# Optimization experiments

Measured on AMD Instinct MI355X. Metric: run time of the kernel, lower is better.

## Reference

```python
import jax, jax.numpy as jnp
import numpy as np

N_NODES = 50000
N_EDGES = 600000
DIM = 128
GROUPS = 32  # min(32, dim)
EPS = 1e-5


def setup_inputs() -> dict:
    key = jax.random.key(0)
    ks = jax.random.split(key, 10)
    src = jax.random.randint(ks[0], (N_EDGES,), 0, N_NODES)
    tgt = jax.random.randint(ks[1], (N_EDGES,), 0, N_NODES)
    # normalized adjacency values (Mtgt): mean aggregation 1/deg(tgt)
    deg = jax.ops.segment_sum(jnp.ones((N_EDGES,), jnp.float32), tgt, num_segments=N_NODES)
    edge_w = 1.0 / jnp.maximum(deg, 1.0)[tgt]
    x = jax.random.normal(ks[2], (N_NODES, DIM), jnp.float32)
    t = jax.random.uniform(ks[3], (), jnp.float32)
    sc = 1.0 / np.sqrt(DIM + 1)
    W1 = jax.random.normal(ks[4], (DIM + 1, DIM), jnp.float32) * sc
    b1 = jax.random.normal(ks[5], (DIM,), jnp.float32) * 0.01
    W2 = jax.random.normal(ks[6], (DIM + 1, DIM), jnp.float32) * sc
    b2 = jax.random.normal(ks[7], (DIM,), jnp.float32) * 0.01
    return {
        "t": t, "x": x, "src": src, "tgt": tgt, "edge_w": edge_w,
        "W1": W1, "b1": b1, "W2": W2, "b2": b2,
        "gamma1": jnp.ones((DIM,), jnp.float32), "beta1": jnp.zeros((DIM,), jnp.float32),
        "gamma2": jnp.ones((DIM,), jnp.float32), "beta2": jnp.zeros((DIM,), jnp.float32),
    }


def _group_norm(h, gamma, beta):
    n, c = h.shape
    hg = h.reshape(n, GROUPS, c // GROUPS)
    mu = hg.mean(axis=-1, keepdims=True)
    var = hg.var(axis=-1, keepdims=True)
    hn = ((hg - mu) * jax.lax.rsqrt(var + EPS)).reshape(n, c)
    return hn * gamma + beta


def _gconv(ttx, W, b, src, tgt, edge_w):
    s = ttx @ W + b                      # [N, dim] projected support
    msg = s[src] * edge_w[:, None]       # [E, dim] gathered, adj-weighted messages
    return jax.ops.segment_sum(msg, tgt, num_segments=N_NODES)


def reference(t, x, src, tgt, edge_w, W1, b1, W2, b2, gamma1, beta1, gamma2, beta2):
    tt = jnp.full((x.shape[0], 1), 1.0, x.dtype) * t
    ttx = jnp.concatenate([tt, x], axis=1)
    h = jax.nn.relu(_gconv(ttx, W1, b1, src, tgt, edge_w))
    h = _group_norm(h, gamma1, beta1)
    ttx = jnp.concatenate([tt, h], axis=1)
    h = jax.nn.relu(_gconv(ttx, W2, b2, src, tgt, edge_w))
    h = _group_norm(h, gamma2, beta2)
    return h
```

## Files before the change

kernel.cpp:

```cpp
#include <hip/hip_runtime.h>
#include <hip/hip_bf16.h>

#define N_NODES 50000
#define N_EDGES 600000
#define DIM 128
#define EPS 1e-5f

#define NPB 64
#define GEMM_GRID ((N_NODES + NPB - 1) / NPB)
#define HIST_BLOCKS 512
#define NSLICE 8
#define GPB 256
#define SCAN_NB 49

typedef float  f32x4   __attribute__((ext_vector_type(4)));
typedef short  s16x8   __attribute__((ext_vector_type(8)));
typedef unsigned short u16x4 __attribute__((ext_vector_type(4)));

__device__ __forceinline__ unsigned short f2b(float f) {
    unsigned int u = __float_as_uint(f);
    return (unsigned short)((u + 0x7fffu + ((u >> 16) & 1u)) >> 16);
}
__device__ __forceinline__ float b2f(unsigned short h) {
    return __uint_as_float(((unsigned int)h) << 16);
}

__device__ __forceinline__ void gemm_body(
    const float* __restrict__ xin, const float* __restrict__ W,
    const float* __restrict__ bias, const float* __restrict__ tptr,
    float* __restrict__ sout, int tile, char* lds)
{
    char* ah = lds;
    char* al = lds + 8192;
    char* wh = lds + 16384;
    char* wl = lds + 32768;

    const int tid  = threadIdx.x;
    const int nb   = tile * NPB;
    const int lane = tid & 63;
    const int wv   = tid >> 6;
    const int g    = lane >> 4;
    const int c16  = lane & 15;

    const float4* xin4 = (const float4*)xin;
    const float4* w4   = (const float4*)(W + DIM);

    f32x4 acc[4][2];
#pragma unroll
    for (int m = 0; m < 4; ++m)
#pragma unroll
        for (int n = 0; n < 2; ++n)
            acc[m][n] = (f32x4){0.f, 0.f, 0.f, 0.f};

#pragma unroll 1
    for (int kt = 0; kt < 2; ++kt) {
        if (kt) __syncthreads();

#pragma unroll
        for (int i = 0; i < 4; ++i) {
            int f4 = tid + i * 256;
            int nl = f4 >> 4;
            int q  = f4 & 15;
            int node = nb + nl;
            float4 v = make_float4(0.f, 0.f, 0.f, 0.f);
            if (node < N_NODES) v = xin4[(size_t)node * 32 + kt * 16 + q];
            unsigned short h0 = f2b(v.x), h1 = f2b(v.y), h2 = f2b(v.z), h3 = f2b(v.w);
            unsigned short l0 = f2b(v.x - b2f(h0)), l1 = f2b(v.y - b2f(h1));
            unsigned short l2 = f2b(v.z - b2f(h2)), l3 = f2b(v.w - b2f(h3));
            int byt = (nl * 128 + q * 8) ^ ((nl & 7) << 4);
            *(u16x4*)(ah + byt) = (u16x4){h0, h1, h2, h3};
            *(u16x4*)(al + byt) = (u16x4){l0, l1, l2, l3};
        }
#pragma unroll
        for (int i = 0; i < 8; ++i) {
            int f4 = tid + i * 256;
            int kr = f4 >> 5;
            int c4 = f4 & 31;
            float4 v = w4[(size_t)(kt * 64 + kr) * 32 + c4];
            unsigned short h0 = f2b(v.x), h1 = f2b(v.y), h2 = f2b(v.z), h3 = f2b(v.w);
            unsigned short l0 = f2b(v.x - b2f(h0)), l1 = f2b(v.y - b2f(h1));
            unsigned short l2 = f2b(v.z - b2f(h2)), l3 = f2b(v.w - b2f(h3));
            int cc = c4 >> 2, cq = c4 & 3;
            int byt = (cc * 2048 + kr * 32 + cq * 8) ^ (((kr >> 3) & 3) << 5);
            *(u16x4*)(wh + byt) = (u16x4){h0, h1, h2, h3};
            *(u16x4*)(wl + byt) = (u16x4){l0, l1, l2, l3};
        }
        __syncthreads();

#pragma unroll
        for (int ks = 0; ks < 2; ++ks) {
            const int k0 = ks * 32;
            s16x8 Ah[4], Al[4];
#pragma unroll
            for (int m = 0; m < 4; ++m) {
                int node = m * 16 + c16;
                int byt = (node * 128 + ks * 64 + g * 16) ^ ((node & 7) << 4);
                Ah[m] = *(const s16x8*)(ah + byt);
                Al[m] = *(const s16x8*)(al + byt);
            }
            s16x8 Bh[2], Bl[2];
#pragma unroll
            for (int n = 0; n < 2; ++n) {
                int cc = wv * 2 + n;
                int sw = ((((k0 >> 3) + g) & 3) << 5);
                int fb = cc * 2048 + (k0 + g * 8) * 32 + c16 * 2;
#pragma unroll
                for (int j = 0; j < 8; ++j) {
                    int a = (fb + j * 32) ^ sw;
                    Bh[n][j] = *(const short*)(wh + a);
                    Bl[n][j] = *(const short*)(wl + a);
                }
            }
#pragma unroll
            for (int m = 0; m < 4; ++m)
#pragma unroll
                for (int n = 0; n < 2; ++n)
                    acc[m][n] = __builtin_amdgcn_mfma_f32_16x16x32_bf16(Ah[m], Bh[n], acc[m][n], 0, 0, 0);
#pragma unroll
            for (int m = 0; m < 4; ++m)
#pragma unroll
                for (int n = 0; n < 2; ++n)
                    acc[m][n] = __builtin_amdgcn_mfma_f32_16x16x32_bf16(Ah[m], Bl[n], acc[m][n], 0, 0, 0);
#pragma unroll
            for (int m = 0; m < 4; ++m)
#pragma unroll
                for (int n = 0; n < 2; ++n)
                    acc[m][n] = __builtin_amdgcn_mfma_f32_16x16x32_bf16(Al[m], Bh[n], acc[m][n], 0, 0, 0);
        }
    }

    const float tval = *tptr;
    float w0[2], bb[2];
#pragma unroll
    for (int n = 0; n < 2; ++n) {
        int c = wv * 32 + n * 16 + c16;
        w0[n] = W[c];
        bb[n] = bias[c];
    }
#pragma unroll
    for (int m = 0; m < 4; ++m) {
        int node0 = nb + m * 16 + g * 4;
#pragma unroll
        for (int n = 0; n < 2; ++n) {
            size_t sbase = (size_t)(wv * 2 + n) * N_NODES * 16 + c16;
#pragma unroll
            for (int r = 0; r < 4; ++r) {
                int nd = node0 + r;
                if (nd < N_NODES)
                    sout[sbase + (size_t)nd * 16] = acc[m][n][r] + tval * w0[n] + bb[n];
            }
        }
    }
}

__global__ __launch_bounds__(256) void gemm_hist_kernel(
    const float* __restrict__ xin, const float* __restrict__ W,
    const float* __restrict__ bias, const float* __restrict__ tptr,
    float* __restrict__ sout,
    const int* __restrict__ tgt, int* __restrict__ cursor)
{
    __shared__ __align__(16) char lds[49152];
    if (blockIdx.x < GEMM_GRID) {
        gemm_body(xin, W, bias, tptr, sout, blockIdx.x, lds);
    } else {
        int e = (blockIdx.x - GEMM_GRID) * 256 + threadIdx.x;
        for (; e < N_EDGES; e += HIST_BLOCKS * 256)
            atomicAdd(&cursor[tgt[e]], 1);
    }
}

__global__ __launch_bounds__(256) void gemm_kernel(
    const float* __restrict__ xin, const float* __restrict__ W,
    const float* __restrict__ bias, const float* __restrict__ tptr,
    float* __restrict__ sout)
{
    __shared__ __align__(16) char lds[49152];
    gemm_body(xin, W, bias, tptr, sout, blockIdx.x, lds);
}

__global__ __launch_bounds__(256) void scan_kernel(
    const int* __restrict__ counts, int* __restrict__ bsum,
    int* __restrict__ bsum2, int* __restrict__ flags,
    int* __restrict__ rowptr)
{
    __shared__ int sh[256];
    __shared__ int amILast;
    __shared__ int sbase;
    const int tid = threadIdx.x;
    const int b = blockIdx.x;
    const int n4 = N_NODES / 4;

    int idx4 = b * 256 + tid;
    int4 c = make_int4(0, 0, 0, 0);
    if (idx4 < n4) c = ((const int4*)counts)[idx4];
    int tsum = c.x + c.y + c.z + c.w;

    sh[tid] = tsum;
    __syncthreads();
#pragma unroll
    for (int off = 1; off < 256; off <<= 1) {
        int v = (tid >= off) ? sh[tid - off] : 0;
        __syncthreads();
        sh[tid] += v;
        __syncthreads();
    }
    int incl = sh[tid];

    if (tid == 0) {
        atomicExch(&bsum[b], sh[255]);
        amILast = (atomicAdd(&flags[0], 1) == SCAN_NB - 1);
    }
    __syncthreads();

    if (amILast) {
        if (tid < 64) {
            int v = (tid < SCAN_NB) ? atomicAdd(&bsum[tid], 0) : 0;
            int incl2 = v;
#pragma unroll
            for (int off = 1; off < 64; off <<= 1) {
                int u = __shfl_up(incl2, off);
                if ((threadIdx.x & 63) >= off) incl2 += u;
            }
            if (tid < SCAN_NB) atomicExch(&bsum2[tid], incl2 - v);
        }
        __syncthreads();
        if (tid == 0) atomicExch(&flags[1], 1);
    }

    if (tid == 0) {
        while (atomicAdd(&flags[1], 0) == 0) __builtin_amdgcn_s_sleep(2);
        sbase = atomicAdd(&bsum2[b], 0);
    }
    __syncthreads();

    int base = sbase + incl - tsum;
    if (idx4 < n4) {
        int4 r;
        r.x = base;
        r.y = base + c.x;
        r.z = r.y + c.y;
        r.w = r.z + c.z;
        ((int4*)rowptr)[idx4] = r;
        if (idx4 == n4 - 1) rowptr[N_NODES] = r.w + c.w;
    }
}

__global__ __launch_bounds__(256) void place_kernel(
    const int* __restrict__ src, const int* __restrict__ tgt,
    const int* __restrict__ rowptr,
    int* __restrict__ cursor, int* __restrict__ eid, int E)
{
    int e = blockIdx.x * 256 + threadIdx.x;
    if (e >= E) return;
    int t = tgt[e];
    int idx = atomicSub(&cursor[t], 1) - 1;
    eid[rowptr[t] + idx] = src[e];
}

__global__ __launch_bounds__(256) void gather_gn_kernel(
    const float4* __restrict__ s_sliced, const int* __restrict__ rowptr,
    const int* __restrict__ eid,
    const float* __restrict__ gamma, const float* __restrict__ beta,
    float* __restrict__ out, int N)
{
    const int slice = blockIdx.x & 7;
    const int sblk  = blockIdx.x >> 3;
    const int wave  = threadIdx.x >> 6;
    const int lane  = threadIdx.x & 63;
    const int nslot = lane >> 2;
    const int qin   = lane & 3;

    const float4* stab = s_sliced + (size_t)slice * N_NODES * 4;
    const int gch = slice * 16 + qin * 4;
    const float4 gm = *(const float4*)&gamma[gch];
    const float4 bt = *(const float4*)&beta[gch];

    const int wslot0  = sblk * 4 + wave;
    const int nwslots = GPB * 4;

    for (int base = wslot0 * 16; base < N; base += nwslots * 16) {
        int node = base + nslot;
        bool valid = node < N;
        int beg = 0, end = 0;
        if (valid) {
            beg = rowptr[node];
            end = rowptr[node + 1];
        }

        float4 acc = make_float4(0.f, 0.f, 0.f, 0.f);
        int e = beg;
        for (; e + 3 < end; e += 4) {
            int s0 = eid[e];
            int s1 = eid[e + 1];
            int s2 = eid[e + 2];
            int s3 = eid[e + 3];
            float4 v0 = stab[(size_t)s0 * 4 + qin];
            float4 v1 = stab[(size_t)s1 * 4 + qin];
            float4 v2 = stab[(size_t)s2 * 4 + qin];
            float4 v3 = stab[(size_t)s3 * 4 + qin];
            acc.x += (v0.x + v1.x) + (v2.x + v3.x);
            acc.y += (v0.y + v1.y) + (v2.y + v3.y);
            acc.z += (v0.z + v1.z) + (v2.z + v3.z);
            acc.w += (v0.w + v1.w) + (v2.w + v3.w);
        }
        for (; e < end; ++e) {
            int s = eid[e];
            float4 v = stab[(size_t)s * 4 + qin];
            acc.x += v.x;
            acc.y += v.y;
            acc.z += v.z;
            acc.w += v.w;
        }

        if (valid) {
            int deg = end - beg;
            float inv = (deg > 0) ? (1.0f / (float)deg) : 0.0f;
            float ax = fmaxf(acc.x * inv, 0.f);
            float ay = fmaxf(acc.y * inv, 0.f);
            float az = fmaxf(acc.z * inv, 0.f);
            float aw = fmaxf(acc.w * inv, 0.f);
            float mu = 0.25f * (ax + ay + az + aw);
            float dx = ax - mu, dy = ay - mu, dz = az - mu, dw = aw - mu;
            float var = 0.25f * (dx * dx + dy * dy + dz * dz + dw * dw);
            float rs = rsqrtf(var + EPS);
            float4 r;
            r.x = dx * rs * gm.x + bt.x;
            r.y = dy * rs * gm.y + bt.y;
            r.z = dz * rs * gm.z + bt.z;
            r.w = dw * rs * gm.w + bt.w;
            *(float4*)&out[(size_t)node * DIM + gch] = r;
        }
    }
}

extern "C" void kernel_launch(void* const* d_in, const int* in_sizes, int n_in,
                              void* d_out, int out_size, void* d_ws, size_t ws_size,
                              hipStream_t stream) {
    const float* t      = (const float*)d_in[0];
    const float* x      = (const float*)d_in[1];
    const int*   src    = (const int*)d_in[2];
    const int*   tgt    = (const int*)d_in[3];
    const float* W1     = (const float*)d_in[5];
    const float* b1     = (const float*)d_in[6];
    const float* W2     = (const float*)d_in[7];
    const float* b2     = (const float*)d_in[8];
    const float* gamma1 = (const float*)d_in[9];
    const float* beta1  = (const float*)d_in[10];
    const float* gamma2 = (const float*)d_in[11];
    const float* beta2  = (const float*)d_in[12];
    float* out = (float*)d_out;

    const size_t NODE_BYTES = (size_t)N_NODES * DIM * sizeof(float);
    char* ws = (char*)d_ws;
    size_t off = 0;
    float4* s_sliced = (float4*)(ws + off); off += NODE_BYTES;
    int*    rowptr   = (int*)(ws + off);    off += ((size_t)N_NODES + 4) * 4;
    off = (off + 255) & ~(size_t)255;
    int*    cursor   = (int*)(ws + off);    off += ((size_t)N_NODES + 64) * 4;
    int*    flags    = cursor + N_NODES;
    off = (off + 255) & ~(size_t)255;
    int*    bsum     = (int*)(ws + off);    off += 64 * 4;
    int*    bsum2    = (int*)(ws + off);    off += 64 * 4;
    off = (off + 255) & ~(size_t)255;
    int*    eid      = (int*)(ws + off);    off += (size_t)N_EDGES * 4;

    const int edge_grid   = (N_EDGES + 255) / 256;
    const int gather_grid = NSLICE * GPB;

    hipMemsetAsync(cursor, 0, ((size_t)N_NODES + 64) * 4, stream);
    gemm_hist_kernel<<<GEMM_GRID + HIST_BLOCKS, 256, 0, stream>>>(
        x, W1, b1, t, (float*)s_sliced, tgt, cursor);
    scan_kernel<<<SCAN_NB, 256, 0, stream>>>(cursor, bsum, bsum2, flags, rowptr);
    place_kernel<<<edge_grid, 256, 0, stream>>>(src, tgt, rowptr, cursor, eid, N_EDGES);
    gather_gn_kernel<<<gather_grid, 256, 0, stream>>>(s_sliced, rowptr, eid, gamma1, beta1, out, N_NODES);
    gemm_kernel<<<GEMM_GRID, 256, 0, stream>>>(out, W2, b2, t, (float*)s_sliced);
    gather_gn_kernel<<<gather_grid, 256, 0, stream>>>(s_sliced, rowptr, eid, gamma2, beta2, out, N_NODES);
}
```

Measured before the change: 275.4 us.

## Pre-split weights to bf16 fragments once and keep them in registers

Adds a small prep kernel that converts W1 and W2 into hi/lo bf16 pairs already laid out as MFMA B fragments. Each GEMM block then loads its B fragments straight into registers from global memory, so it no longer converts W per block or stages it through LDS. The x tile is now staged in one full-K pass with a single barrier, and LDS use drops from 48KB to 32KB. In exchange the kernel holds more vector registers for the B fragments and adds an extra kernel launch.

```diff
diff --git a/kernel.cpp b/kernel.cpp
--- a/kernel.cpp
+++ b/kernel.cpp
@@ -25,15 +25,41 @@
     return __uint_as_float(((unsigned int)h) << 16);
 }
 
+__global__ __launch_bounds__(256) void prep_kernel(
+    const float* __restrict__ W1, const float* __restrict__ W2,
+    short* __restrict__ wb1h, short* __restrict__ wb1l,
+    short* __restrict__ wb2h, short* __restrict__ wb2l)
+{
+    const int layer = blockIdx.x >> 3;
+    const int fid = (blockIdx.x & 7) * 256 + threadIdx.x;
+    const int lane = fid & 63;
+    const int ck = fid >> 6;
+    const int k0 = (ck & 3) * 32 + (lane >> 4) * 8;
+    const int c  = (ck >> 2) * 16 + (lane & 15);
+    const float* Wsrc = layer ? W2 : W1;
+    short* dh = layer ? wb2h : wb1h;
+    short* dl = layer ? wb2l : wb1l;
+    s16x8 h, l;
+#pragma unroll
+    for (int j = 0; j < 8; ++j) {
+        float v = Wsrc[(k0 + j + 1) * DIM + c];
+        unsigned short hh = f2b(v);
+        h[j] = (short)hh;
+        l[j] = (short)f2b(v - b2f(hh));
+    }
+    *(s16x8*)(dh + (size_t)fid * 8) = h;
+    *(s16x8*)(dl + (size_t)fid * 8) = l;
+}
+
 __device__ __forceinline__ void gemm_body(
-    const float* __restrict__ xin, const float* __restrict__ W,
-    const float* __restrict__ bias, const float* __restrict__ tptr,
+    const float* __restrict__ xin,
+    const short* __restrict__ wbh, const short* __restrict__ wbl,
+    const float* __restrict__ W, const float* __restrict__ bias,
+    const float* __restrict__ tptr,
     float* __restrict__ sout, int tile, char* lds)
 {
     char* ah = lds;
-    char* al = lds + 8192;
-    char* wh = lds + 16384;
-    char* wl = lds + 32768;
+    char* al = lds + 16384;
 
     const int tid  = threadIdx.x;
     const int nb   = tile * NPB;
@@ -42,8 +68,35 @@
     const int g    = lane >> 4;
     const int c16  = lane & 15;
 
+    s16x8 Bh[2][4], Bl[2][4];
+#pragma unroll
+    for (int n = 0; n < 2; ++n) {
+        int cc = wv * 2 + n;
+#pragma unroll
+        for (int ks = 0; ks < 4; ++ks) {
+            size_t fi = (size_t)((cc * 4 + ks) * 64 + lane) * 8;
+            Bh[n][ks] = *(const s16x8*)(wbh + fi);
+            Bl[n][ks] = *(const s16x8*)(wbl + fi);
+        }
+    }
+
     const float4* xin4 = (const float4*)xin;
-    const float4* w4   = (const float4*)(W + DIM);
+#pragma unroll
+    for (int i = 0; i < 8; ++i) {
+        int f4 = tid + i * 256;
+        int nl = f4 >> 5;
+        int q  = f4 & 31;
+        int node = nb + nl;
+        float4 v = make_float4(0.f, 0.f, 0.f, 0.f);
+        if (node < N_NODES) v = xin4[(size_t)node * 32 + q];
+        unsigned short h0 = f2b(v.x), h1 = f2b(v.y), h2 = f2b(v.z), h3 = f2b(v.w);
+        unsigned short l0 = f2b(v.x - b2f(h0)), l1 = f2b(v.y - b2f(h1));
+        unsigned short l2 = f2b(v.z - b2f(h2)), l3 = f2b(v.w - b2f(h3));
+        int byt = (nl * 256 + q * 8) ^ ((nl & 7) << 4);
+        *(u16x4*)(ah + byt) = (u16x4){h0, h1, h2, h3};
+        *(u16x4*)(al + byt) = (u16x4){l0, l1, l2, l3};
+    }
+    __syncthreads();
 
     f32x4 acc[4][2];
 #pragma unroll
@@ -52,81 +105,34 @@
         for (int n = 0; n < 2; ++n)
             acc[m][n] = (f32x4){0.f, 0.f, 0.f, 0.f};
 
-#pragma unroll 1
-    for (int kt = 0; kt < 2; ++kt) {
-        if (kt) __syncthreads();
-
-#pragma unroll
-        for (int i = 0; i < 4; ++i) {
-            int f4 = tid + i * 256;
-            int nl = f4 >> 4;
-            int q  = f4 & 15;
-            int node = nb + nl;
-            float4 v = make_float4(0.f, 0.f, 0.f, 0.f);
-            if (node < N_NODES) v = xin4[(size_t)node * 32 + kt * 16 + q];
-            unsigned short h0 = f2b(v.x), h1 = f2b(v.y), h2 = f2b(v.z), h3 = f2b(v.w);
-            unsigned short l0 = f2b(v.x - b2f(h0)), l1 = f2b(v.y - b2f(h1));
-            unsigned short l2 = f2b(v.z - b2f(h2)), l3 = f2b(v.w - b2f(h3));
-            int byt = (nl * 128 + q * 8) ^ ((nl & 7) << 4);
-            *(u16x4*)(ah + byt) = (u16x4){h0, h1, h2, h3};
-            *(u16x4*)(al + byt) = (u16x4){l0, l1, l2, l3};
-        }
-#pragma unroll
-        for (int i = 0; i < 8; ++i) {
-            int f4 = tid + i * 256;
-            int kr = f4 >> 5;
-            int c4 = f4 & 31;
-            float4 v = w4[(size_t)(kt * 64 + kr) * 32 + c4];
-            unsigned short h0 = f2b(v.x), h1 = f2b(v.y), h2 = f2b(v.z), h3 = f2b(v.w);
-            unsigned short l0 = f2b(v.x - b2f(h0)), l1 = f2b(v.y - b2f(h1));
-            unsigned short l2 = f2b(v.z - b2f(h2)), l3 = f2b(v.w - b2f(h3));
-            int cc = c4 >> 2, cq = c4 & 3;
-            int byt = (cc * 2048 + kr * 32 + cq * 8) ^ (((kr >> 3) & 3) << 5);
-            *(u16x4*)(wh + byt) = (u16x4){h0, h1, h2, h3};
-            *(u16x4*)(wl + byt) = (u16x4){l0, l1, l2, l3};
-        }
-        __syncthreads();
-
-#pragma unroll
-        for (int ks = 0; ks < 2; ++ks) {
-            const int k0 = ks * 32;
-            s16x8 Ah[4], Al[4];
-#pragma unroll
-            for (int m = 0; m < 4; ++m) {
-                int node = m * 16 + c16;
-                int byt = (node * 128 + ks * 64 + g * 16) ^ ((node & 7) << 4);
-                Ah[m] = *(const s16x8*)(ah + byt);
-                Al[m] = *(const s16x8*)(al + byt);
+#pragma unroll
+    for (int ks = 0; ks < 4; ++ks) {
+        s16x8 Ah[4];
+#pragma unroll
+        for (int m = 0; m < 4; ++m) {
+            int node = m * 16 + c16;
+            int byt = (node * 256 + ks * 64 + g * 16) ^ ((node & 7) << 4);
+            Ah[m] = *(const s16x8*)(ah + byt);
+        }
+#pragma unroll
+        for (int m = 0; m < 4; ++m)
+#pragma unroll
+            for (int n = 0; n < 2; ++n) {
+                acc[m][n] = __builtin_amdgcn_mfma_f32_16x16x32_bf16(Ah[m], Bh[n][ks], acc[m][n], 0, 0, 0);
+                acc[m][n] = __builtin_amdgcn_mfma_f32_16x16x32_bf16(Ah[m], Bl[n][ks], acc[m][n], 0, 0, 0);
             }
-            s16x8 Bh[2], Bl[2];
-#pragma unroll
-            for (int n = 0; n < 2; ++n) {
-                int cc = wv * 2 + n;
-                int sw = ((((k0 >> 3) + g) & 3) << 5);
-                int fb = cc * 2048 + (k0 + g * 8) * 32 + c16 * 2;
-#pragma unroll
-                for (int j = 0; j < 8; ++j) {
-                    int a = (fb + j * 32) ^ sw;
-                    Bh[n][j] = *(const short*)(wh + a);
-                    Bl[n][j] = *(const short*)(wl + a);
-                }
-            }
-#pragma unroll
-            for (int m = 0; m < 4; ++m)
-#pragma unroll
-                for (int n = 0; n < 2; ++n)
-                    acc[m][n] = __builtin_amdgcn_mfma_f32_16x16x32_bf16(Ah[m], Bh[n], acc[m][n], 0, 0, 0);
-#pragma unroll
-            for (int m = 0; m < 4; ++m)
-#pragma unroll
-                for (int n = 0; n < 2; ++n)
-                    acc[m][n] = __builtin_amdgcn_mfma_f32_16x16x32_bf16(Ah[m], Bl[n], acc[m][n], 0, 0, 0);
-#pragma unroll
-            for (int m = 0; m < 4; ++m)
-#pragma unroll
-                for (int n = 0; n < 2; ++n)
-                    acc[m][n] = __builtin_amdgcn_mfma_f32_16x16x32_bf16(Al[m], Bh[n], acc[m][n], 0, 0, 0);
-        }
+        s16x8 Alo[4];
+#pragma unroll
+        for (int m = 0; m < 4; ++m) {
+            int node = m * 16 + c16;
+            int byt = (node * 256 + ks * 64 + g * 16) ^ ((node & 7) << 4);
+            Alo[m] = *(const s16x8*)(al + byt);
+        }
+#pragma unroll
+        for (int m = 0; m < 4; ++m)
+#pragma unroll
+            for (int n = 0; n < 2; ++n)
+                acc[m][n] = __builtin_amdgcn_mfma_f32_16x16x32_bf16(Alo[m], Bh[n][ks], acc[m][n], 0, 0, 0);
     }
 
     const float tval = *tptr;
@@ -154,14 +160,15 @@
 }
 
 __global__ __launch_bounds__(256) void gemm_hist_kernel(
-    const float* __restrict__ xin, const float* __restrict__ W,
-    const float* __restrict__ bias, const float* __restrict__ tptr,
-    float* __restrict__ sout,
+    const float* __restrict__ xin,
+    const short* __restrict__ wbh, const short* __restrict__ wbl,
+    const float* __restrict__ W, const float* __restrict__ bias,
+    const float* __restrict__ tptr, float* __restrict__ sout,
     const int* __restrict__ tgt, int* __restrict__ cursor)
 {
-    __shared__ __align__(16) char lds[49152];
+    __shared__ __align__(16) char lds[32768];
     if (blockIdx.x < GEMM_GRID) {
-        gemm_body(xin, W, bias, tptr, sout, blockIdx.x, lds);
+        gemm_body(xin, wbh, wbl, W, bias, tptr, sout, blockIdx.x, lds);
     } else {
         int e = (blockIdx.x - GEMM_GRID) * 256 + threadIdx.x;
         for (; e < N_EDGES; e += HIST_BLOCKS * 256)
@@ -170,12 +177,13 @@
 }
 
 __global__ __launch_bounds__(256) void gemm_kernel(
-    const float* __restrict__ xin, const float* __restrict__ W,
-    const float* __restrict__ bias, const float* __restrict__ tptr,
-    float* __restrict__ sout)
-{
-    __shared__ __align__(16) char lds[49152];
-    gemm_body(xin, W, bias, tptr, sout, blockIdx.x, lds);
+    const float* __restrict__ xin,
+    const short* __restrict__ wbh, const short* __restrict__ wbl,
+    const float* __restrict__ W, const float* __restrict__ bias,
+    const float* __restrict__ tptr, float* __restrict__ sout)
+{
+    __shared__ __align__(16) char lds[32768];
+    gemm_body(xin, wbh, wbl, W, bias, tptr, sout, blockIdx.x, lds);
 }
 
 __global__ __launch_bounds__(256) void scan_kernel(
@@ -363,16 +371,22 @@
     int*    bsum2    = (int*)(ws + off);    off += 64 * 4;
     off = (off + 255) & ~(size_t)255;
     int*    eid      = (int*)(ws + off);    off += (size_t)N_EDGES * 4;
+    off = (off + 255) & ~(size_t)255;
+    short*  wb1h     = (short*)(ws + off);  off += 16384 * 2;
+    short*  wb1l     = (short*)(ws + off);  off += 16384 * 2;
+    short*  wb2h     = (short*)(ws + off);  off += 16384 * 2;
+    short*  wb2l     = (short*)(ws + off);  off += 16384 * 2;
 
     const int edge_grid   = (N_EDGES + 255) / 256;
     const int gather_grid = NSLICE * GPB;
 
+    prep_kernel<<<16, 256, 0, stream>>>(W1, W2, wb1h, wb1l, wb2h, wb2l);
     hipMemsetAsync(cursor, 0, ((size_t)N_NODES + 64) * 4, stream);
     gemm_hist_kernel<<<GEMM_GRID + HIST_BLOCKS, 256, 0, stream>>>(
-        x, W1, b1, t, (float*)s_sliced, tgt, cursor);
+        x, wb1h, wb1l, W1, b1, t, (float*)s_sliced, tgt, cursor);
     scan_kernel<<<SCAN_NB, 256, 0, stream>>>(cursor, bsum, bsum2, flags, rowptr);
     place_kernel<<<edge_grid, 256, 0, stream>>>(src, tgt, rowptr, cursor, eid, N_EDGES);
     gather_gn_kernel<<<gather_grid, 256, 0, stream>>>(s_sliced, rowptr, eid, gamma1, beta1, out, N_NODES);
-    gemm_kernel<<<GEMM_GRID, 256, 0, stream>>>(out, W2, b2, t, (float*)s_sliced);
+    gemm_kernel<<<GEMM_GRID, 256, 0, stream>>>(out, wb2h, wb2l, W2, b2, t, (float*)s_sliced);
     gather_gn_kernel<<<gather_grid, 256, 0, stream>>>(s_sliced, rowptr, eid, gamma2, beta2, out, N_NODES);
 }
```

New measurement: 268.5 us. 1.03x faster.
